# Performance work log

Measured on AMD Instinct MI355X. Metric: run time of the kernel, lower is better.

## Reference

```python
import jax, jax.numpy as jnp
import numpy as np

N_HEAD = 16


def setup_inputs() -> dict:
    key = jax.random.key(0)
    k1, k2, k3 = jax.random.split(key, 3)
    B, T, C = 4, 2048, 2048
    x = jax.random.normal(k1, (B, T, C), dtype=jnp.float32)
    # GPT-style small init so attention logits are in a sane range
    W_attn = jax.random.normal(k2, (3 * C, C), dtype=jnp.float32) * 0.02
    W_proj = jax.random.normal(k3, (C, C), dtype=jnp.float32) * 0.02
    return {"x": x, "W_attn": W_attn, "W_proj": W_proj}


def reference(x, W_attn, W_proj):
    B, T, C = x.shape
    H = N_HEAD
    d = C // H
    # c_attn: eqx.nn.Linear(weight [3C, C]) applied per-token -> x @ W_attn.T
    qkv = jnp.einsum('btc,fc->btf', x, W_attn)  # [B, T, 3C]
    q, k, v = jnp.split(qkv, 3, axis=-1)
    q = q.reshape(B, T, H, d).transpose(0, 2, 1, 3)  # [B, H, T, d]
    k = k.reshape(B, T, H, d).transpose(0, 2, 1, 3)
    v = v.reshape(B, T, H, d).transpose(0, 2, 1, 3)
    att = jnp.einsum('bhqd,bhkd->bhqk', q, k)  # [B, H, T, T]
    # causal mask: positions j > i are masked (future tokens)
    causal = jnp.tril(jnp.ones((T, T), dtype=bool))
    att = jnp.where(causal, att, -jnp.inf)
    att = jax.nn.softmax(att / jnp.sqrt(jnp.asarray(d, att.dtype)), axis=-1)
    out = jnp.einsum('bhqk,bhkd->bhqd', att, v)  # [B, H, T, d]
    out = out.transpose(0, 2, 1, 3).reshape(B, T, C)
    # c_proj -> out @ W_proj.T
    return jnp.einsum('btc,oc->bto', out, W_proj)
```

## Files before the change

### kernel.cpp

```cpp
#include <hip/hip_runtime.h>
#include <hip/hip_bf16.h>
#include <stdint.h>

typedef __hip_bfloat16 bf16;
typedef __attribute__((ext_vector_type(8))) __bf16 bf16x8;
typedef __attribute__((ext_vector_type(8))) unsigned short ushort8;
typedef __attribute__((ext_vector_type(4))) float floatx4;

#define MFMA_16x16x32(a, b, c) __builtin_amdgcn_mfma_f32_16x16x32_bf16((a), (b), (c), 0, 0, 0)

__device__ __forceinline__ void async_load16(const bf16* g, bf16* l) {
  __builtin_amdgcn_global_load_lds(
      (const __attribute__((address_space(1))) unsigned int*)g,
      (__attribute__((address_space(3))) unsigned int*)l,
      16, 0, 0);
}

template <int CTRL>
__device__ __forceinline__ float dpp_f(float x) {
  return __builtin_bit_cast(float, __builtin_amdgcn_update_dpp(
      0, __builtin_bit_cast(int, x), CTRL, 0xf, 0xf, true));
}
__device__ __forceinline__ float row_max16(float x) {
  x = fmaxf(x, dpp_f<0xB1>(x));
  x = fmaxf(x, dpp_f<0x4E>(x));
  x = fmaxf(x, dpp_f<0x124>(x));
  x = fmaxf(x, dpp_f<0x128>(x));
  return x;
}
__device__ __forceinline__ float row_sum16(float x) {
  x += dpp_f<0xB1>(x);
  x += dpp_f<0x4E>(x);
  x += dpp_f<0x124>(x);
  x += dpp_f<0x128>(x);
  return x;
}

__global__ __launch_bounds__(256)
void f32_to_bf16_k(const float* __restrict__ in, bf16* __restrict__ out, int n)
{
  const int i = (blockIdx.x * 256 + threadIdx.x) * 8;
  if (i >= n) return;
  bf16 tmp[8];
#pragma unroll
  for (int j = 0; j < 8; ++j) tmp[j] = __float2bfloat16(in[i + j]);
  *(ushort8*)&out[i] = *(const ushort8*)tmp;
}

__global__ __launch_bounds__(256, 2)
void gemm_bt(const bf16* __restrict__ A, const bf16* __restrict__ B,
             bf16* __restrict__ Cb, float* __restrict__ Cf,
             int M, int N, int K)
{
  __shared__ __align__(16) bf16 sA[2][128 * 32];
  __shared__ __align__(16) bf16 sB[2][128 * 32];

  const int tid  = threadIdx.x;
  const int lane = tid & 63;
  const int w    = tid >> 6;
  const int wm   = w >> 1;
  const int wn   = w & 1;
  const int quad = lane >> 4;
  const int l16  = lane & 15;
  const int tileM = blockIdx.y * 128;
  const int tileN = blockIdx.x * 128;
  const int rmask = (l16 & 3) ^ ((l16 >> 2) & 3);

  floatx4 acc[4][4];
#pragma unroll
  for (int i = 0; i < 4; ++i)
#pragma unroll
    for (int j = 0; j < 4; ++j) acc[i][j] = (floatx4){0.f, 0.f, 0.f, 0.f};

  int st_row[2], st_col[2];
#pragma unroll
  for (int s = 0; s < 2; ++s) {
    const int cid = (w * 2 + s) * 64 + lane;
    const int row = cid >> 2;
    st_row[s] = row;
    st_col[s] = ((cid & 3) ^ ((row & 3) ^ ((row >> 2) & 3))) << 3;
  }

#pragma unroll
  for (int s = 0; s < 2; ++s) {
    async_load16(A + (size_t)(tileM + st_row[s]) * K + st_col[s], &sA[0][(w * 2 + s) * 512]);
    async_load16(B + (size_t)(tileN + st_row[s]) * K + st_col[s], &sB[0][(w * 2 + s) * 512]);
  }

  int p = 0;
  for (int k0 = 0; k0 < K; k0 += 32, p ^= 1) {
    __syncthreads();
    if (k0 + 32 < K) {
#pragma unroll
      for (int s = 0; s < 2; ++s) {
        async_load16(A + (size_t)(tileM + st_row[s]) * K + (k0 + 32) + st_col[s], &sA[p ^ 1][(w * 2 + s) * 512]);
        async_load16(B + (size_t)(tileN + st_row[s]) * K + (k0 + 32) + st_col[s], &sB[p ^ 1][(w * 2 + s) * 512]);
      }
    }

    bf16x8 af[4], bfr[4];
#pragma unroll
    for (int i = 0; i < 4; ++i)
      af[i] = *(const bf16x8*)&sA[p][(wm * 64 + i * 16 + l16) * 32 + (quad ^ rmask) * 8];
#pragma unroll
    for (int j = 0; j < 4; ++j)
      bfr[j] = *(const bf16x8*)&sB[p][(wn * 64 + j * 16 + l16) * 32 + (quad ^ rmask) * 8];
#pragma unroll
    for (int i = 0; i < 4; ++i)
#pragma unroll
      for (int j = 0; j < 4; ++j)
        acc[i][j] = MFMA_16x16x32(af[i], bfr[j], acc[i][j]);
  }

#pragma unroll
  for (int i = 0; i < 4; ++i)
#pragma unroll
    for (int j = 0; j < 4; ++j)
#pragma unroll
      for (int r = 0; r < 4; ++r) {
        const int row = tileM + wm * 64 + i * 16 + quad * 4 + r;
        const int col = tileN + wn * 64 + j * 16 + l16;
        if (Cf) Cf[(size_t)row * N + col] = acc[i][j][r];
        else    Cb[(size_t)row * N + col] = __float2bfloat16(acc[i][j][r]);
      }
}

__global__ __launch_bounds__(256)
void transpose_v(const bf16* __restrict__ qkv, bf16* __restrict__ Vt)
{
  __shared__ bf16 tile[64 * 128];
  const int t0 = blockIdx.x * 64;
  const int bh = blockIdx.y;
  const int b = bh >> 4;
  const int h = bh & 15;
  const int tid = threadIdx.x;
  const bf16* src = qkv + (size_t)(b * 2048 + t0) * 6144 + 4096 + h * 128;
#pragma unroll
  for (int s = 0; s < 4; ++s) {
    const int cid = s * 256 + tid;
    const int row = cid >> 4;
    const int col = (cid & 15) << 3;
    *(ushort8*)&tile[row * 128 + col] = *(const ushort8*)&src[(size_t)row * 6144 + col];
  }
  __syncthreads();
  const int dim = tid >> 1;
  const int tp  = (tid & 1) << 5;
  bf16 vals[32];
#pragma unroll
  for (int t = 0; t < 32; ++t) vals[t] = tile[(tp + t) * 128 + dim];
  bf16* dst = Vt + (size_t)(bh * 128 + dim) * 2048 + t0 + tp;
#pragma unroll
  for (int s = 0; s < 4; ++s) *(ushort8*)&dst[s * 8] = ((const ushort8*)vals)[s];
}

__global__ __launch_bounds__(256, 2)
void flash_attn(const bf16* __restrict__ qkv, const bf16* __restrict__ Vt,
                bf16* __restrict__ outb)
{
  __shared__ __align__(16) bf16 smem[16384 + 4 * 32 * 40];
  bf16* sP = smem + 16384;

  const int qb  = gridDim.y - 1 - blockIdx.y;
  const int bh  = blockIdx.x;
  const int b   = bh >> 4;
  const int h   = bh & 15;
  const int tid = threadIdx.x;
  const int lane = tid & 63;
  const int w    = tid >> 6;
  const int quad = lane >> 4;
  const int l16  = lane & 15;

  const size_t rs = 6144;
  const bf16* Qg = qkv + (size_t)(b * 2048 + qb * 128) * rs + h * 128;
  const bf16* Kg = qkv + (size_t)(b * 2048) * rs + 2048 + h * 128;
  const bf16* Vg = Vt + (size_t)bh * 128 * 2048;

#pragma unroll
  for (int s = 0; s < 8; ++s) {
    const int cid = (w * 8 + s) * 64 + lane;
    const int row = cid >> 4;
    const int col = ((cid & 15) ^ (row & 15)) << 3;
    async_load16(Qg + (size_t)row * rs + col, &smem[(w * 8 + s) * 512]);
  }
  __syncthreads();

  bf16x8 qf[2][4];
#pragma unroll
  for (int i = 0; i < 2; ++i)
#pragma unroll
    for (int kc = 0; kc < 4; ++kc)
      qf[i][kc] = *(const bf16x8*)&smem[(w * 32 + i * 16 + l16) * 128 + (((kc * 4 + quad) ^ l16) << 3)];
  __syncthreads();

  int kq_row[2], kq_col[2], vv_row[2], vv_col[2];
#pragma unroll
  for (int s = 0; s < 2; ++s) {
    const int cid = (w * 2 + s) * 64 + lane;
    kq_row[s] = cid >> 4;
    kq_col[s] = ((cid & 15) ^ (kq_row[s] & 15)) << 3;
    vv_row[s] = cid >> 2;
    vv_col[s] = ((cid & 3) ^ (vv_row[s] & 3)) << 3;
  }

  const int kb_end = 4 * qb + 4;
#pragma unroll
  for (int s = 0; s < 2; ++s) {
    async_load16(Kg + (size_t)kq_row[s] * rs + kq_col[s],      &smem[(w * 2 + s) * 512]);
    async_load16(Vg + (size_t)vv_row[s] * 2048 + vv_col[s],    &smem[4096 + (w * 2 + s) * 512]);
  }

  floatx4 o[2][8];
#pragma unroll
  for (int i = 0; i < 2; ++i)
#pragma unroll
    for (int s = 0; s < 8; ++s) o[i][s] = (floatx4){0.f, 0.f, 0.f, 0.f};
  float m_i[2][4], l_i[2][4];
#pragma unroll
  for (int i = 0; i < 2; ++i)
#pragma unroll
    for (int r = 0; r < 4; ++r) { m_i[i][r] = -__builtin_inff(); l_i[i][r] = 0.f; }

  const float csc = 1.4426950408889634f * 0.08838834764831845f;

  for (int kb = 0; kb < kb_end; ++kb) {
    __syncthreads();
    if (kb + 1 < kb_end) {
      bf16* nb = smem + ((kb + 1) & 1) * 8192;
#pragma unroll
      for (int s = 0; s < 2; ++s) {
        async_load16(Kg + (size_t)((kb + 1) * 32 + kq_row[s]) * rs + kq_col[s], nb + (w * 2 + s) * 512);
        async_load16(Vg + (size_t)vv_row[s] * 2048 + (kb + 1) * 32 + vv_col[s], nb + 4096 + (w * 2 + s) * 512);
      }
    }
    if (kb * 32 > qb * 128 + w * 32 + 31) continue;

    const bf16* sK = smem + (kb & 1) * 8192;
    const bf16* sV = sK + 4096;

    floatx4 sacc[2][2];
#pragma unroll
    for (int i = 0; i < 2; ++i)
#pragma unroll
      for (int j = 0; j < 2; ++j) sacc[i][j] = (floatx4){0.f, 0.f, 0.f, 0.f};
#pragma unroll
    for (int kc = 0; kc < 4; ++kc) {
      const int ch = ((kc * 4 + quad) ^ l16) << 3;
#pragma unroll
      for (int j = 0; j < 2; ++j) {
        const bf16x8 bk = *(const bf16x8*)&sK[(j * 16 + l16) * 128 + ch];
        sacc[0][j] = MFMA_16x16x32(qf[0][kc], bk, sacc[0][j]);
        sacc[1][j] = MFMA_16x16x32(qf[1][kc], bk, sacc[1][j]);
      }
    }

    const bool diag = (kb * 32 + 31 > qb * 128 + w * 32);
    float p[2][2][4];
#pragma unroll
    for (int i = 0; i < 2; ++i) {
      const int qrow = qb * 128 + w * 32 + i * 16 + quad * 4;
#pragma unroll
      for (int r = 0; r < 4; ++r) {
        float mx = -__builtin_inff();
#pragma unroll
        for (int j = 0; j < 2; ++j) {
          float v = sacc[i][j][r] * csc;
          if (diag && kb * 32 + j * 16 + l16 > qrow + r) v = -__builtin_inff();
          p[i][j][r] = v;
          mx = fmaxf(mx, v);
        }
        mx = row_max16(mx);
        const float mnew = fmaxf(m_i[i][r], mx);
        const float alpha = __builtin_amdgcn_exp2f(m_i[i][r] - mnew);
        m_i[i][r] = mnew;
        float rsl = 0.f;
#pragma unroll
        for (int j = 0; j < 2; ++j) {
          const float e = __builtin_amdgcn_exp2f(p[i][j][r] - mnew);
          p[i][j][r] = e;
          rsl += e;
        }
        l_i[i][r] = alpha * l_i[i][r] + row_sum16(rsl);
#pragma unroll
        for (int s = 0; s < 8; ++s) o[i][s][r] *= alpha;
      }
    }

#pragma unroll
    for (int i = 0; i < 2; ++i)
#pragma unroll
      for (int j = 0; j < 2; ++j)
#pragma unroll
        for (int r = 0; r < 4; ++r)
          sP[w * 1280 + (i * 16 + quad * 4 + r) * 40 + j * 16 + l16] = __float2bfloat16(p[i][j][r]);

    const bf16x8 ap0 = *(const bf16x8*)&sP[w * 1280 + l16 * 40 + quad * 8];
    const bf16x8 ap1 = *(const bf16x8*)&sP[w * 1280 + (16 + l16) * 40 + quad * 8];
    const int chv = (quad ^ (l16 & 3)) << 3;
#pragma unroll
    for (int s = 0; s < 8; ++s) {
      const bf16x8 bv = *(const bf16x8*)&sV[(s * 16 + l16) * 32 + chv];
      o[0][s] = MFMA_16x16x32(ap0, bv, o[0][s]);
      o[1][s] = MFMA_16x16x32(ap1, bv, o[1][s]);
    }
  }

#pragma unroll
  for (int i = 0; i < 2; ++i) {
    float rl[4];
#pragma unroll
    for (int r = 0; r < 4; ++r) rl[r] = 1.f / l_i[i][r];
    bf16* dst = outb + (size_t)(b * 2048 + qb * 128 + w * 32 + i * 16) * 2048 + h * 128;
#pragma unroll
    for (int s = 0; s < 8; ++s)
#pragma unroll
      for (int r = 0; r < 4; ++r)
        dst[(size_t)(quad * 4 + r) * 2048 + s * 16 + l16] = __float2bfloat16(o[i][s][r] * rl[r]);
  }
}

extern "C" void kernel_launch(void* const* d_in, const int* in_sizes, int n_in,
                              void* d_out, int out_size, void* d_ws, size_t ws_size,
                              hipStream_t stream)
{
  (void)in_sizes; (void)n_in; (void)out_size; (void)ws_size;
  const float* x  = (const float*)d_in[0];
  const float* Wa = (const float*)d_in[1];
  const float* Wp = (const float*)d_in[2];
  float* out = (float*)d_out;
  char* ws = (char*)d_ws;

  bf16* xb   = (bf16*)(ws + 0);
  bf16* Wab  = (bf16*)(ws + 33554432ull);
  bf16* Wpb  = (bf16*)(ws + 58720256ull);
  bf16* qkv  = (bf16*)(ws + 67108864ull);
  bf16* attb = (bf16*)(ws + 167772160ull);
  bf16* Vt   = xb;

  f32_to_bf16_k<<<8192, 256, 0, stream>>>(x,  xb,  4 * 2048 * 2048);
  f32_to_bf16_k<<<6144, 256, 0, stream>>>(Wa, Wab, 3 * 2048 * 2048);
  f32_to_bf16_k<<<2048, 256, 0, stream>>>(Wp, Wpb, 2048 * 2048);

  gemm_bt<<<dim3(48, 64), 256, 0, stream>>>(xb, Wab, qkv, nullptr, 8192, 6144, 2048);
  transpose_v<<<dim3(32, 64), 256, 0, stream>>>(qkv, Vt);
  flash_attn<<<dim3(64, 16), 256, 0, stream>>>(qkv, Vt, attb);
  gemm_bt<<<dim3(16, 64), 256, 0, stream>>>(attb, Wpb, nullptr, out, 8192, 2048, 2048);
}
```

Measured before the change: 640.1 us.

## Rewrite GEMM with 256x256 tiles, 8 waves, split-phase pipeline and XCD remap

Replaces the 128x128x32 double-buffered GEMM with a 256x256x64 tile run by 512 threads. Loads are split into half-tile stages interleaved with MFMA phases, using explicit vmcnt waits and raw barriers, plus setprio around the MFMA blocks. Block IDs are remapped across the 8 XCDs to improve L2 locality. The goal is higher arithmetic intensity and better overlap of global-to-LDS loads with compute. In exchange, LDS use (128KB) and register pressure grow a lot, and correctness depends on the vmcnt accounting being right.

```diff
diff --git a/kernel.cpp b/kernel.cpp
--- a/kernel.cpp
+++ b/kernel.cpp
@@ -47,82 +47,139 @@
   *(ushort8*)&out[i] = *(const ushort8*)tmp;
 }
 
-__global__ __launch_bounds__(256, 2)
+#define G_BAR __builtin_amdgcn_s_barrier()
+
+#define G_STAGE(pg, ls, tt, h)                                                  \
+  do {                                                                          \
+    async_load16((pg) + (size_t)((h) * 64) * K + (size_t)(tt) * 64,             \
+                 (ls) + (h) * 4096 + lws);                                      \
+    async_load16((pg) + (size_t)((h) * 64 + 128) * K + (size_t)(tt) * 64,       \
+                 (ls) + (h) * 4096 + 8192 + lws);                               \
+  } while (0)
+
+#define G_RD_A(mh)                                                              \
+  _Pragma("unroll") for (int i = 0; i < 4; ++i) {                               \
+    const int rb = (wm * 128 + (mh) * 64 + i * 16 + l16) * 64;                  \
+    af[i][0] = *(const bf16x8*)&sAd[rb + ach0];                                 \
+    af[i][1] = *(const bf16x8*)&sAd[rb + ach1];                                 \
+  }
+
+#define G_RD_B(dst, nh)                                                         \
+  _Pragma("unroll") for (int j = 0; j < 2; ++j) {                               \
+    const int rb = (wn * 64 + (nh) * 32 + j * 16 + l16) * 64;                   \
+    dst[j][0] = *(const bf16x8*)&sBd[rb + ach0];                                \
+    dst[j][1] = *(const bf16x8*)&sBd[rb + ach1];                                \
+  }
+
+#define G_MM(mh, nh, BF)                                                        \
+  __builtin_amdgcn_s_setprio(1);                                                \
+  _Pragma("unroll") for (int kk = 0; kk < 2; ++kk)                              \
+  _Pragma("unroll") for (int i = 0; i < 4; ++i)                                 \
+  _Pragma("unroll") for (int j = 0; j < 2; ++j)                                 \
+    acc[(mh) * 4 + i][(nh) * 2 + j] =                                           \
+        MFMA_16x16x32(af[i][kk], BF[j][kk], acc[(mh) * 4 + i][(nh) * 2 + j]);   \
+  __builtin_amdgcn_s_setprio(0);
+
+__global__ __launch_bounds__(512, 2)
 void gemm_bt(const bf16* __restrict__ A, const bf16* __restrict__ B,
              bf16* __restrict__ Cb, float* __restrict__ Cf,
              int M, int N, int K)
 {
-  __shared__ __align__(16) bf16 sA[2][128 * 32];
-  __shared__ __align__(16) bf16 sB[2][128 * 32];
+  __shared__ __align__(16) bf16 sA[2][256 * 64];
+  __shared__ __align__(16) bf16 sB[2][256 * 64];
 
   const int tid  = threadIdx.x;
   const int lane = tid & 63;
   const int w    = tid >> 6;
-  const int wm   = w >> 1;
-  const int wn   = w & 1;
+  const int wm   = w >> 2;
+  const int wn   = w & 3;
   const int quad = lane >> 4;
   const int l16  = lane & 15;
-  const int tileM = blockIdx.y * 128;
-  const int tileN = blockIdx.x * 128;
-  const int rmask = (l16 & 3) ^ ((l16 >> 2) & 3);
-
-  floatx4 acc[4][4];
-#pragma unroll
-  for (int i = 0; i < 4; ++i)
+
+  const int nbx = N >> 8;
+  const int nwg = nbx * (M >> 8);
+  const int wg  = (blockIdx.x & 7) * (nwg >> 3) + (blockIdx.x >> 3);
+  const int tileM = (wg / nbx) << 8;
+  const int tileN = (wg % nbx) << 8;
+
+  const int srow = tid >> 3;
+  const int scol = ((tid & 7) ^ (srow & 7)) << 3;
+  const bf16* pA = A + (size_t)(tileM + srow) * K + scol;
+  const bf16* pB = B + (size_t)(tileN + srow) * K + scol;
+  const int lws = w * 512;
+
+  const int ach0 = ((quad ^ (l16 & 7)) << 3);
+  const int ach1 = (((4 + quad) ^ (l16 & 7)) << 3);
+
+  floatx4 acc[8][4];
+#pragma unroll
+  for (int i = 0; i < 8; ++i)
 #pragma unroll
     for (int j = 0; j < 4; ++j) acc[i][j] = (floatx4){0.f, 0.f, 0.f, 0.f};
 
-  int st_row[2], st_col[2];
-#pragma unroll
-  for (int s = 0; s < 2; ++s) {
-    const int cid = (w * 2 + s) * 64 + lane;
-    const int row = cid >> 2;
-    st_row[s] = row;
-    st_col[s] = ((cid & 3) ^ ((row & 3) ^ ((row >> 2) & 3))) << 3;
-  }
-
-#pragma unroll
-  for (int s = 0; s < 2; ++s) {
-    async_load16(A + (size_t)(tileM + st_row[s]) * K + st_col[s], &sA[0][(w * 2 + s) * 512]);
-    async_load16(B + (size_t)(tileN + st_row[s]) * K + st_col[s], &sB[0][(w * 2 + s) * 512]);
-  }
-
-  int p = 0;
-  for (int k0 = 0; k0 < K; k0 += 32, p ^= 1) {
-    __syncthreads();
-    if (k0 + 32 < K) {
-#pragma unroll
-      for (int s = 0; s < 2; ++s) {
-        async_load16(A + (size_t)(tileM + st_row[s]) * K + (k0 + 32) + st_col[s], &sA[p ^ 1][(w * 2 + s) * 512]);
-        async_load16(B + (size_t)(tileN + st_row[s]) * K + (k0 + 32) + st_col[s], &sB[p ^ 1][(w * 2 + s) * 512]);
-      }
-    }
-
-    bf16x8 af[4], bfr[4];
-#pragma unroll
-    for (int i = 0; i < 4; ++i)
-      af[i] = *(const bf16x8*)&sA[p][(wm * 64 + i * 16 + l16) * 32 + (quad ^ rmask) * 8];
-#pragma unroll
-    for (int j = 0; j < 4; ++j)
-      bfr[j] = *(const bf16x8*)&sB[p][(wn * 64 + j * 16 + l16) * 32 + (quad ^ rmask) * 8];
-#pragma unroll
-    for (int i = 0; i < 4; ++i)
-#pragma unroll
-      for (int j = 0; j < 4; ++j)
-        acc[i][j] = MFMA_16x16x32(af[i], bfr[j], acc[i][j]);
-  }
-
-#pragma unroll
-  for (int i = 0; i < 4; ++i)
-#pragma unroll
-    for (int j = 0; j < 4; ++j)
-#pragma unroll
-      for (int r = 0; r < 4; ++r) {
-        const int row = tileM + wm * 64 + i * 16 + quad * 4 + r;
-        const int col = tileN + wn * 64 + j * 16 + l16;
-        if (Cf) Cf[(size_t)row * N + col] = acc[i][j][r];
-        else    Cb[(size_t)row * N + col] = __float2bfloat16(acc[i][j][r]);
-      }
+  const int T = K >> 6;
+
+  G_STAGE(pA, &sA[0][0], 0, 0);
+  G_STAGE(pB, &sB[0][0], 0, 0);
+  G_STAGE(pB, &sB[0][0], 0, 1);
+  G_STAGE(pA, &sA[0][0], 0, 1);
+  if (T > 1) {
+    G_STAGE(pA, &sA[1][0], 1, 0);
+    G_STAGE(pB, &sB[1][0], 1, 0);
+    asm volatile("s_waitcnt vmcnt(4)" ::: "memory");
+  } else {
+    asm volatile("s_waitcnt vmcnt(0)" ::: "memory");
+  }
+  G_BAR;
+
+  bf16x8 af[4][2], bf0[2][2], bf1[2][2];
+  for (int t = 0; t < T; ++t) {
+    const bf16* sAd = &sA[t & 1][0];
+    const bf16* sBd = &sB[t & 1][0];
+    bf16* sAn = &sA[(t + 1) & 1][0];
+    bf16* sBn = &sB[(t + 1) & 1][0];
+    bf16* sAc = &sA[t & 1][0];
+    bf16* sBc = &sB[t & 1][0];
+
+    G_RD_A(0); G_RD_B(bf0, 0);
+    if (t + 1 < T) G_STAGE(pB, sBn, t + 1, 1);
+    G_BAR; G_MM(0, 0, bf0); G_BAR;
+
+    G_RD_B(bf1, 1);
+    if (t + 1 < T) G_STAGE(pA, sAn, t + 1, 1);
+    G_BAR; G_MM(0, 1, bf1); G_BAR;
+
+    G_RD_A(1);
+    if (t + 2 < T) G_STAGE(pA, sAc, t + 2, 0);
+    G_BAR; G_MM(1, 0, bf0); G_BAR;
+
+    if (t + 2 < T) G_STAGE(pB, sBc, t + 2, 0);
+    G_BAR; G_MM(1, 1, bf1);
+    if (t + 2 < T) asm volatile("s_waitcnt vmcnt(4)" ::: "memory");
+    else           asm volatile("s_waitcnt vmcnt(0)" ::: "memory");
+    G_BAR;
+  }
+
+  const int orow = tileM + wm * 128 + quad * 4;
+  const int ocol = tileN + wn * 64 + l16;
+  if (Cf) {
+#pragma unroll
+    for (int fm = 0; fm < 8; ++fm)
+#pragma unroll
+      for (int fn = 0; fn < 4; ++fn)
+#pragma unroll
+        for (int r = 0; r < 4; ++r)
+          Cf[(size_t)(orow + fm * 16 + r) * N + ocol + fn * 16] = acc[fm][fn][r];
+  } else {
+#pragma unroll
+    for (int fm = 0; fm < 8; ++fm)
+#pragma unroll
+      for (int fn = 0; fn < 4; ++fn)
+#pragma unroll
+        for (int r = 0; r < 4; ++r)
+          Cb[(size_t)(orow + fm * 16 + r) * N + ocol + fn * 16] =
+              __float2bfloat16(acc[fm][fn][r]);
+  }
 }
 
 __global__ __launch_bounds__(256)
@@ -340,8 +397,8 @@
   f32_to_bf16_k<<<6144, 256, 0, stream>>>(Wa, Wab, 3 * 2048 * 2048);
   f32_to_bf16_k<<<2048, 256, 0, stream>>>(Wp, Wpb, 2048 * 2048);
 
-  gemm_bt<<<dim3(48, 64), 256, 0, stream>>>(xb, Wab, qkv, nullptr, 8192, 6144, 2048);
+  gemm_bt<<<dim3(768), 512, 0, stream>>>(xb, Wab, qkv, nullptr, 8192, 6144, 2048);
   transpose_v<<<dim3(32, 64), 256, 0, stream>>>(qkv, Vt);
   flash_attn<<<dim3(64, 16), 256, 0, stream>>>(qkv, Vt, attb);
-  gemm_bt<<<dim3(16, 64), 256, 0, stream>>>(attb, Wpb, nullptr, out, 8192, 2048, 2048);
-}
+  gemm_bt<<<dim3(256), 512, 0, stream>>>(attb, Wpb, nullptr, out, 8192, 2048, 2048);
+}
```

Measured after the change: 577.0 us. 1.11x faster.
